# Kernel optimization log

Measured on AMD Instinct MI355X. Metric: run time of the kernel, lower is better.

The kernel has to match this reference:

```python
import jax, jax.numpy as jnp
import numpy as np

B = 1024      # batch of samples accumulated
F_DIM = 768   # backbone feature dim (ViT out_dim)
M = 512       # buffer_size (random projection width)
C = 100       # number of classes


def setup_inputs() -> dict:
    key = jax.random.key(0)
    k1, k2, k3 = jax.random.split(key, 3)
    X = jax.random.normal(k1, (B, F_DIM), dtype=jnp.float32)
    # RandomBuffer weight (fixed random projection), Linear-style init scale
    W = jax.random.normal(k2, (F_DIM, M), dtype=jnp.float32) / np.float32(np.sqrt(F_DIM))
    labels = jax.random.randint(k3, (B,), 0, C)  # argmax(Y, dim=1)
    return {"X": X, "W": W, "labels": labels}


def reference(X, W, labels):
    # RandomBuffer.forward: relu(X @ W) -> [B, M]
    feat = jax.nn.relu(X @ W)
    # per-sample outer product f^T f, scatter-added per class label
    outer = feat[:, :, None] * feat[:, None, :]          # [B, M, M]
    phi = jax.ops.segment_sum(outer, labels, num_segments=C)   # [C, M, M]
    mu = jax.ops.segment_sum(feat, labels, num_segments=C)     # [C, M]
    count = jax.ops.segment_sum(jnp.ones((B,), feat.dtype), labels, num_segments=C)  # [C]
    return phi, mu, count
```

## Files before the change

### kernel.cpp

```cpp
#include <hip/hip_runtime.h>

#define B_N    1024
#define F_DIMC 768
#define M_DIM  512
#define C_N    100
#define KHALF  (F_DIMC / 2)
#define NT2    (KHALF / 32)
#define NGEMM  512
#define NIDX   25

typedef float f32x4 __attribute__((ext_vector_type(4)));

__global__ __launch_bounds__(256) void gemm_index_kernel(
    const float* __restrict__ X, const float* __restrict__ W,
    const int* __restrict__ labels, float* __restrict__ part,
    int* __restrict__ counts, int* __restrict__ idx) {
  __shared__ float As[2][32][36];
  __shared__ float Bs[2][32][64];
  __shared__ int   lab[B_N];

  const int t = threadIdx.x;

  if (blockIdx.x >= NGEMM) {
    for (int i = t; i < B_N; i += 256) lab[i] = labels[i];
    __syncthreads();
    const int w    = t >> 6;
    const int lane = t & 63;
    const int c    = ((int)blockIdx.x - NGEMM) * 4 + w;
    if (c < C_N) {
      int base = 0;
      for (int ch = 0; ch < 16; ++ch) {
        const int j = ch * 64 + lane;
        const bool hit = (lab[j] == c);
        const unsigned long long mask = __ballot(hit);
        if (hit) {
          const int r = __popcll(mask & ((1ull << lane) - 1ull));
          idx[c * B_N + base + r] = j;
        }
        base += __popcll(mask);
      }
      if (lane == 0) counts[c] = base;
    }
    return;
  }

  const int kb   = (int)blockIdx.x >> 8;
  const int tile = (int)blockIdx.x & 255;
  const int bm = (tile >> 3) * 32;
  const int bn = (tile & 7) * 64;
  const int tx = t & 15;
  const int ty = t >> 4;

  const int ar  = t >> 3;
  const int akq = (t & 7) * 4;
  const int bk0 = t >> 4;
  const int bk1 = bk0 + 16;
  const int bnq = (t & 15) * 4;

  const float* __restrict__ Arow =
      X + (size_t)(bm + ar) * F_DIMC + kb * KHALF + akq;
  const float* __restrict__ Bcol =
      W + (size_t)kb * KHALF * M_DIM + bn + bnq;

  float4 pa  = *(const float4*)(Arow);
  float4 pb0 = *(const float4*)(Bcol + (size_t)bk0 * M_DIM);
  float4 pb1 = *(const float4*)(Bcol + (size_t)bk1 * M_DIM);

  float acc[2][4] = {};

  As[0][akq + 0][ar] = pa.x;
  As[0][akq + 1][ar] = pa.y;
  As[0][akq + 2][ar] = pa.z;
  As[0][akq + 3][ar] = pa.w;
  *(float4*)&Bs[0][bk0][bnq] = pb0;
  *(float4*)&Bs[0][bk1][bnq] = pb1;
  __syncthreads();

  for (int it = 0; it < NT2; ++it) {
    const int cur = it & 1;
    if (it + 1 < NT2) {
      const int k0 = (it + 1) * 32;
      pa  = *(const float4*)(Arow + k0);
      pb0 = *(const float4*)(Bcol + (size_t)(k0 + bk0) * M_DIM);
      pb1 = *(const float4*)(Bcol + (size_t)(k0 + bk1) * M_DIM);
    }
#pragma unroll
    for (int kk = 0; kk < 32; ++kk) {
      float2 av = *(const float2*)&As[cur][kk][ty * 2];
      float4 bv = *(const float4*)&Bs[cur][kk][tx * 4];
      acc[0][0] += av.x * bv.x;
      acc[0][1] += av.x * bv.y;
      acc[0][2] += av.x * bv.z;
      acc[0][3] += av.x * bv.w;
      acc[1][0] += av.y * bv.x;
      acc[1][1] += av.y * bv.y;
      acc[1][2] += av.y * bv.z;
      acc[1][3] += av.y * bv.w;
    }
    if (it + 1 < NT2) {
      const int nxt = cur ^ 1;
      As[nxt][akq + 0][ar] = pa.x;
      As[nxt][akq + 1][ar] = pa.y;
      As[nxt][akq + 2][ar] = pa.z;
      As[nxt][akq + 3][ar] = pa.w;
      *(float4*)&Bs[nxt][bk0][bnq] = pb0;
      *(float4*)&Bs[nxt][bk1][bnq] = pb1;
    }
    __syncthreads();
  }

  float* __restrict__ dst = part + (size_t)kb * B_N * M_DIM;
#pragma unroll
  for (int j = 0; j < 2; ++j) {
    float4 o = make_float4(acc[j][0], acc[j][1], acc[j][2], acc[j][3]);
    *(float4*)&dst[(size_t)(bm + ty * 2 + j) * M_DIM + bn + tx * 4] = o;
  }
}

__global__ __launch_bounds__(256, 4) void phi_mu_kernel(
    const float* __restrict__ p0, const float* __restrict__ p1,
    const int* __restrict__ counts, const int* __restrict__ idx,
    float* __restrict__ phi, float* __restrict__ mu,
    float* __restrict__ cnt_out) {
  const int c = blockIdx.y;
  const int n = counts[c];
  const int* __restrict__ id = idx + c * B_N;
  const int t = threadIdx.x;

  if (blockIdx.x == 16) {
    float2 acc = make_float2(0.f, 0.f);
    for (int s = 0; s < n; ++s) {
      const size_t o = (size_t)id[s] * M_DIM + t * 2;
      const float2 q0 = *(const float2*)&p0[o];
      const float2 q1 = *(const float2*)&p1[o];
      acc.x += fmaxf(q0.x + q1.x, 0.f);
      acc.y += fmaxf(q0.y + q1.y, 0.f);
    }
    *(float2*)&mu[(size_t)c * M_DIM + t * 2] = acc;
    if (t == 0) cnt_out[c] = (float)n;
    return;
  }

  const int px = (int)blockIdx.x;
  const int tr = t >> 6;
  const int tc = t & 63;

  __shared__ float F[16][M_DIM];

  float acc[8][8] = {};

  for (int s0 = 0; s0 < n; s0 += 16) {
    const int chunk  = min(16, n - s0);
    if (s0) __syncthreads();
    const int nslots = chunk << 7;
    for (int v = t; v < nslots; v += 256) {
      const int sl   = v >> 7;
      const int fp   = (v & 127) << 2;
      const size_t o = (size_t)id[s0 + sl] * M_DIM + fp;
      const float4 q0 = *(const float4*)&p0[o];
      const float4 q1 = *(const float4*)&p1[o];
      float4 f;
      f.x = fmaxf(q0.x + q1.x, 0.f);
      f.y = fmaxf(q0.y + q1.y, 0.f);
      f.z = fmaxf(q0.z + q1.z, 0.f);
      f.w = fmaxf(q0.w + q1.w, 0.f);
      *(float4*)&F[sl][fp] = f;
    }
    __syncthreads();
    for (int sl = 0; sl < chunk; ++sl) {
      const float4 a0 = *(const float4*)&F[sl][px * 32 + tr * 8];
      const float4 a1 = *(const float4*)&F[sl][px * 32 + tr * 8 + 4];
      const float4 b0 = *(const float4*)&F[sl][tc * 4];
      const float4 b1 = *(const float4*)&F[sl][256 + tc * 4];
      const float av[8] = {a0.x, a0.y, a0.z, a0.w, a1.x, a1.y, a1.z, a1.w};
      const float bv[8] = {b0.x, b0.y, b0.z, b0.w, b1.x, b1.y, b1.z, b1.w};
#pragma unroll
      for (int r = 0; r < 8; ++r)
#pragma unroll
        for (int q = 0; q < 8; ++q)
          acc[r][q] += av[r] * bv[q];
    }
  }

  float* __restrict__ out = phi + (size_t)c * M_DIM * M_DIM;
#pragma unroll
  for (int r = 0; r < 8; ++r) {
    const size_t row = (size_t)(px * 32 + tr * 8 + r) * M_DIM;
    const f32x4 o0 = {acc[r][0], acc[r][1], acc[r][2], acc[r][3]};
    const f32x4 o1 = {acc[r][4], acc[r][5], acc[r][6], acc[r][7]};
    __builtin_nontemporal_store(o0, (f32x4*)&out[row + tc * 4]);
    __builtin_nontemporal_store(o1, (f32x4*)&out[row + 256 + tc * 4]);
  }
}

extern "C" void kernel_launch(void* const* d_in, const int* in_sizes, int n_in,
                              void* d_out, int out_size, void* d_ws,
                              size_t ws_size, hipStream_t stream) {
  const float* X      = (const float*)d_in[0];
  const float* W      = (const float*)d_in[1];
  const int*   labels = (const int*)d_in[2];

  float* out = (float*)d_out;
  float* phi = out;
  float* mu  = out + (size_t)C_N * M_DIM * M_DIM;
  float* cnt = mu + (size_t)C_N * M_DIM;

  float* part   = (float*)d_ws;
  int*   counts = (int*)((char*)d_ws + (size_t)2 * B_N * M_DIM * sizeof(float));
  int*   idx    = counts + 128;

  hipLaunchKernelGGL(gemm_index_kernel, dim3(NGEMM + NIDX), dim3(256), 0,
                     stream, X, W, labels, part, counts, idx);
  hipLaunchKernelGGL(phi_mu_kernel, dim3(17, C_N), dim3(256), 0, stream,
                     part, part + (size_t)B_N * M_DIM, counts, idx,
                     phi, mu, cnt);
}
```

Baseline: 47.24 us.

## Merge split-K partials with atomics and enlarge phi blocks to 1024 threads

The two split-K GEMM halves now accumulate into a single zeroed buffer via float atomics, so the phi/mu kernel reads one partial instead of two. The buffer is cleared with a memset before the GEMM. The phi kernel is regrouped into 1024-thread blocks, each covering four 32-row strips, so every gathered sample chunk staged in LDS serves four times as many output rows. The nontemporal stores for phi are replaced by plain stores. This adds a memset, atomic traffic and fewer, larger blocks (5x100 grid), which may hurt occupancy and latency hiding.

New measurement: 60.39 us. 1.28x slower.

```diff
diff --git a/kernel.cpp b/kernel.cpp
--- a/kernel.cpp
+++ b/kernel.cpp
@@ -8,8 +8,6 @@
 #define NT2    (KHALF / 32)
 #define NGEMM  512
 #define NIDX   25
-
-typedef float f32x4 __attribute__((ext_vector_type(4)));
 
 __global__ __launch_bounds__(256) void gemm_index_kernel(
     const float* __restrict__ X, const float* __restrict__ W,
@@ -109,67 +107,64 @@
     __syncthreads();
   }
 
-  float* __restrict__ dst = part + (size_t)kb * B_N * M_DIM;
 #pragma unroll
   for (int j = 0; j < 2; ++j) {
-    float4 o = make_float4(acc[j][0], acc[j][1], acc[j][2], acc[j][3]);
-    *(float4*)&dst[(size_t)(bm + ty * 2 + j) * M_DIM + bn + tx * 4] = o;
+    float* __restrict__ d = part + (size_t)(bm + ty * 2 + j) * M_DIM + bn + tx * 4;
+    unsafeAtomicAdd(d + 0, acc[j][0]);
+    unsafeAtomicAdd(d + 1, acc[j][1]);
+    unsafeAtomicAdd(d + 2, acc[j][2]);
+    unsafeAtomicAdd(d + 3, acc[j][3]);
   }
 }
 
-__global__ __launch_bounds__(256, 4) void phi_mu_kernel(
-    const float* __restrict__ p0, const float* __restrict__ p1,
-    const int* __restrict__ counts, const int* __restrict__ idx,
-    float* __restrict__ phi, float* __restrict__ mu,
-    float* __restrict__ cnt_out) {
+__global__ __launch_bounds__(1024, 1) void phi_mu_kernel(
+    const float* __restrict__ part, const int* __restrict__ counts,
+    const int* __restrict__ idx, float* __restrict__ phi,
+    float* __restrict__ mu, float* __restrict__ cnt_out) {
   const int c = blockIdx.y;
   const int n = counts[c];
   const int* __restrict__ id = idx + c * B_N;
   const int t = threadIdx.x;
 
-  if (blockIdx.x == 16) {
-    float2 acc = make_float2(0.f, 0.f);
-    for (int s = 0; s < n; ++s) {
-      const size_t o = (size_t)id[s] * M_DIM + t * 2;
-      const float2 q0 = *(const float2*)&p0[o];
-      const float2 q1 = *(const float2*)&p1[o];
-      acc.x += fmaxf(q0.x + q1.x, 0.f);
-      acc.y += fmaxf(q0.y + q1.y, 0.f);
-    }
-    *(float2*)&mu[(size_t)c * M_DIM + t * 2] = acc;
+  if (blockIdx.x == 4) {
+    if (t < M_DIM) {
+      float a = 0.f;
+      for (int s = 0; s < n; ++s)
+        a += fmaxf(part[(size_t)id[s] * M_DIM + t], 0.f);
+      mu[(size_t)c * M_DIM + t] = a;
+    }
     if (t == 0) cnt_out[c] = (float)n;
     return;
   }
 
-  const int px = (int)blockIdx.x;
-  const int tr = t >> 6;
+  const int tp = t >> 8;
+  const int tr = (t >> 6) & 3;
   const int tc = t & 63;
+  const int prow = ((int)blockIdx.x * 4 + tp) * 32 + tr * 8;
 
   __shared__ float F[16][M_DIM];
 
   float acc[8][8] = {};
 
   for (int s0 = 0; s0 < n; s0 += 16) {
-    const int chunk  = min(16, n - s0);
+    const int chunk = min(16, n - s0);
     if (s0) __syncthreads();
     const int nslots = chunk << 7;
-    for (int v = t; v < nslots; v += 256) {
-      const int sl   = v >> 7;
-      const int fp   = (v & 127) << 2;
-      const size_t o = (size_t)id[s0 + sl] * M_DIM + fp;
-      const float4 q0 = *(const float4*)&p0[o];
-      const float4 q1 = *(const float4*)&p1[o];
+    for (int v = t; v < nslots; v += 1024) {
+      const int sl = v >> 7;
+      const int fp = (v & 127) << 2;
+      const float4 q = *(const float4*)&part[(size_t)id[s0 + sl] * M_DIM + fp];
       float4 f;
-      f.x = fmaxf(q0.x + q1.x, 0.f);
-      f.y = fmaxf(q0.y + q1.y, 0.f);
-      f.z = fmaxf(q0.z + q1.z, 0.f);
-      f.w = fmaxf(q0.w + q1.w, 0.f);
+      f.x = fmaxf(q.x, 0.f);
+      f.y = fmaxf(q.y, 0.f);
+      f.z = fmaxf(q.z, 0.f);
+      f.w = fmaxf(q.w, 0.f);
       *(float4*)&F[sl][fp] = f;
     }
     __syncthreads();
     for (int sl = 0; sl < chunk; ++sl) {
-      const float4 a0 = *(const float4*)&F[sl][px * 32 + tr * 8];
-      const float4 a1 = *(const float4*)&F[sl][px * 32 + tr * 8 + 4];
+      const float4 a0 = *(const float4*)&F[sl][prow];
+      const float4 a1 = *(const float4*)&F[sl][prow + 4];
       const float4 b0 = *(const float4*)&F[sl][tc * 4];
       const float4 b1 = *(const float4*)&F[sl][256 + tc * 4];
       const float av[8] = {a0.x, a0.y, a0.z, a0.w, a1.x, a1.y, a1.z, a1.w};
@@ -185,11 +180,11 @@
   float* __restrict__ out = phi + (size_t)c * M_DIM * M_DIM;
 #pragma unroll
   for (int r = 0; r < 8; ++r) {
-    const size_t row = (size_t)(px * 32 + tr * 8 + r) * M_DIM;
-    const f32x4 o0 = {acc[r][0], acc[r][1], acc[r][2], acc[r][3]};
-    const f32x4 o1 = {acc[r][4], acc[r][5], acc[r][6], acc[r][7]};
-    __builtin_nontemporal_store(o0, (f32x4*)&out[row + tc * 4]);
-    __builtin_nontemporal_store(o1, (f32x4*)&out[row + 256 + tc * 4]);
+    const size_t row = (size_t)(prow + r) * M_DIM;
+    *(float4*)&out[row + tc * 4] =
+        make_float4(acc[r][0], acc[r][1], acc[r][2], acc[r][3]);
+    *(float4*)&out[row + 256 + tc * 4] =
+        make_float4(acc[r][4], acc[r][5], acc[r][6], acc[r][7]);
   }
 }
 
@@ -206,12 +201,12 @@
   float* cnt = mu + (size_t)C_N * M_DIM;
 
   float* part   = (float*)d_ws;
-  int*   counts = (int*)((char*)d_ws + (size_t)2 * B_N * M_DIM * sizeof(float));
+  int*   counts = (int*)((char*)d_ws + (size_t)B_N * M_DIM * sizeof(float));
   int*   idx    = counts + 128;
 
+  hipMemsetAsync(part, 0, (size_t)B_N * M_DIM * sizeof(float), stream);
   hipLaunchKernelGGL(gemm_index_kernel, dim3(NGEMM + NIDX), dim3(256), 0,
                      stream, X, W, labels, part, counts, idx);
-  hipLaunchKernelGGL(phi_mu_kernel, dim3(17, C_N), dim3(256), 0, stream,
-                     part, part + (size_t)B_N * M_DIM, counts, idx,
-                     phi, mu, cnt);
+  hipLaunchKernelGGL(phi_mu_kernel, dim3(5, C_N), dim3(1024), 0, stream,
+                     part, counts, idx, phi, mu, cnt);
 }
```

## Split GEMM K four ways with 64x64 tiles and halve phi staging chunk

Applied to the files above, without the earlier changes.

The projection GEMM now splits K into four partial sums instead of two and uses 64x64 output tiles with a 4x4 register micro-tile per thread, keeping the block count at 512. The phi/mu kernel then reads and sums four partial buffers before the ReLU, and stages 8 samples per chunk instead of 16 to cut shared-memory use. The phi output stores change from nontemporal to ordinary stores. This gives more register reuse in the GEMM, but the second kernel reads twice as much partial data and synchronises more often.

New measurement: 48.83 us. 1.03x slower.

```diff
diff --git a/kernel.cpp b/kernel.cpp
--- a/kernel.cpp
+++ b/kernel.cpp
@@ -4,18 +4,17 @@
 #define F_DIMC 768
 #define M_DIM  512
 #define C_N    100
-#define KHALF  (F_DIMC / 2)
-#define NT2    (KHALF / 32)
+#define KSPLIT 4
+#define KPER   (F_DIMC / KSPLIT)
+#define NBK    (KPER / 32)
 #define NGEMM  512
 #define NIDX   25
-
-typedef float f32x4 __attribute__((ext_vector_type(4)));
 
 __global__ __launch_bounds__(256) void gemm_index_kernel(
     const float* __restrict__ X, const float* __restrict__ W,
     const int* __restrict__ labels, float* __restrict__ part,
     int* __restrict__ counts, int* __restrict__ idx) {
-  __shared__ float As[2][32][36];
+  __shared__ float As[2][32][68];
   __shared__ float Bs[2][32][64];
   __shared__ int   lab[B_N];
 
@@ -44,81 +43,88 @@
     return;
   }
 
-  const int kb   = (int)blockIdx.x >> 8;
-  const int tile = (int)blockIdx.x & 255;
-  const int bm = (tile >> 3) * 32;
+  const int kb   = (int)blockIdx.x >> 7;
+  const int tile = (int)blockIdx.x & 127;
+  const int bm = (tile >> 3) * 64;
   const int bn = (tile & 7) * 64;
-  const int tx = t & 15;
-  const int ty = t >> 4;
-
-  const int ar  = t >> 3;
-  const int akq = (t & 7) * 4;
-  const int bk0 = t >> 4;
-  const int bk1 = bk0 + 16;
-  const int bnq = (t & 15) * 4;
-
-  const float* __restrict__ Arow =
-      X + (size_t)(bm + ar) * F_DIMC + kb * KHALF + akq;
-  const float* __restrict__ Bcol =
-      W + (size_t)kb * KHALF * M_DIM + bn + bnq;
-
-  float4 pa  = *(const float4*)(Arow);
-  float4 pb0 = *(const float4*)(Bcol + (size_t)bk0 * M_DIM);
-  float4 pb1 = *(const float4*)(Bcol + (size_t)bk1 * M_DIM);
-
-  float acc[2][4] = {};
-
-  As[0][akq + 0][ar] = pa.x;
-  As[0][akq + 1][ar] = pa.y;
-  As[0][akq + 2][ar] = pa.z;
-  As[0][akq + 3][ar] = pa.w;
-  *(float4*)&Bs[0][bk0][bnq] = pb0;
-  *(float4*)&Bs[0][bk1][bnq] = pb1;
+  const int tr = t >> 4;
+  const int tc = t & 15;
+
+  const int ar0 = t >> 3,          akq0 = (t & 7) * 4;
+  const int ar1 = (t + 256) >> 3,  akq1 = (t & 7) * 4;
+  const int bkr0 = t >> 4,         bnq0 = (t & 15) * 4;
+  const int bkr1 = (t + 256) >> 4, bnq1 = (t & 15) * 4;
+
+  const float* __restrict__ Xb = X + (size_t)bm * F_DIMC + kb * KPER;
+  const float* __restrict__ Wb = W + (size_t)kb * KPER * M_DIM + bn;
+
+  float4 pa0 = *(const float4*)&Xb[(size_t)ar0 * F_DIMC + akq0];
+  float4 pa1 = *(const float4*)&Xb[(size_t)ar1 * F_DIMC + akq1];
+  float4 pb0 = *(const float4*)&Wb[(size_t)bkr0 * M_DIM + bnq0];
+  float4 pb1 = *(const float4*)&Wb[(size_t)bkr1 * M_DIM + bnq1];
+
+  float acc[4][4] = {};
+
+  As[0][akq0 + 0][ar0] = pa0.x;
+  As[0][akq0 + 1][ar0] = pa0.y;
+  As[0][akq0 + 2][ar0] = pa0.z;
+  As[0][akq0 + 3][ar0] = pa0.w;
+  As[0][akq1 + 0][ar1] = pa1.x;
+  As[0][akq1 + 1][ar1] = pa1.y;
+  As[0][akq1 + 2][ar1] = pa1.z;
+  As[0][akq1 + 3][ar1] = pa1.w;
+  *(float4*)&Bs[0][bkr0][bnq0] = pb0;
+  *(float4*)&Bs[0][bkr1][bnq1] = pb1;
   __syncthreads();
 
-  for (int it = 0; it < NT2; ++it) {
+  for (int it = 0; it < NBK; ++it) {
     const int cur = it & 1;
-    if (it + 1 < NT2) {
+    if (it + 1 < NBK) {
       const int k0 = (it + 1) * 32;
-      pa  = *(const float4*)(Arow + k0);
-      pb0 = *(const float4*)(Bcol + (size_t)(k0 + bk0) * M_DIM);
-      pb1 = *(const float4*)(Bcol + (size_t)(k0 + bk1) * M_DIM);
+      pa0 = *(const float4*)&Xb[(size_t)ar0 * F_DIMC + k0 + akq0];
+      pa1 = *(const float4*)&Xb[(size_t)ar1 * F_DIMC + k0 + akq1];
+      pb0 = *(const float4*)&Wb[(size_t)(k0 + bkr0) * M_DIM + bnq0];
+      pb1 = *(const float4*)&Wb[(size_t)(k0 + bkr1) * M_DIM + bnq1];
     }
 #pragma unroll
     for (int kk = 0; kk < 32; ++kk) {
-      float2 av = *(const float2*)&As[cur][kk][ty * 2];
-      float4 bv = *(const float4*)&Bs[cur][kk][tx * 4];
-      acc[0][0] += av.x * bv.x;
-      acc[0][1] += av.x * bv.y;
-      acc[0][2] += av.x * bv.z;
-      acc[0][3] += av.x * bv.w;
-      acc[1][0] += av.y * bv.x;
-      acc[1][1] += av.y * bv.y;
-      acc[1][2] += av.y * bv.z;
-      acc[1][3] += av.y * bv.w;
-    }
-    if (it + 1 < NT2) {
+      const float4 a = *(const float4*)&As[cur][kk][tr * 4];
+      const float4 b = *(const float4*)&Bs[cur][kk][tc * 4];
+      const float av[4] = {a.x, a.y, a.z, a.w};
+      const float bv[4] = {b.x, b.y, b.z, b.w};
+#pragma unroll
+      for (int j = 0; j < 4; ++j)
+#pragma unroll
+        for (int q = 0; q < 4; ++q)
+          acc[j][q] += av[j] * bv[q];
+    }
+    if (it + 1 < NBK) {
       const int nxt = cur ^ 1;
-      As[nxt][akq + 0][ar] = pa.x;
-      As[nxt][akq + 1][ar] = pa.y;
-      As[nxt][akq + 2][ar] = pa.z;
-      As[nxt][akq + 3][ar] = pa.w;
-      *(float4*)&Bs[nxt][bk0][bnq] = pb0;
-      *(float4*)&Bs[nxt][bk1][bnq] = pb1;
+      As[nxt][akq0 + 0][ar0] = pa0.x;
+      As[nxt][akq0 + 1][ar0] = pa0.y;
+      As[nxt][akq0 + 2][ar0] = pa0.z;
+      As[nxt][akq0 + 3][ar0] = pa0.w;
+      As[nxt][akq1 + 0][ar1] = pa1.x;
+      As[nxt][akq1 + 1][ar1] = pa1.y;
+      As[nxt][akq1 + 2][ar1] = pa1.z;
+      As[nxt][akq1 + 3][ar1] = pa1.w;
+      *(float4*)&Bs[nxt][bkr0][bnq0] = pb0;
+      *(float4*)&Bs[nxt][bkr1][bnq1] = pb1;
     }
     __syncthreads();
   }
 
   float* __restrict__ dst = part + (size_t)kb * B_N * M_DIM;
 #pragma unroll
-  for (int j = 0; j < 2; ++j) {
-    float4 o = make_float4(acc[j][0], acc[j][1], acc[j][2], acc[j][3]);
-    *(float4*)&dst[(size_t)(bm + ty * 2 + j) * M_DIM + bn + tx * 4] = o;
+  for (int j = 0; j < 4; ++j) {
+    *(float4*)&dst[(size_t)(bm + tr * 4 + j) * M_DIM + bn + tc * 4] =
+        make_float4(acc[j][0], acc[j][1], acc[j][2], acc[j][3]);
   }
 }
 
 __global__ __launch_bounds__(256, 4) void phi_mu_kernel(
     const float* __restrict__ p0, const float* __restrict__ p1,
+    const float* __restrict__ p2, const float* __restrict__ p3,
     const int* __restrict__ counts, const int* __restrict__ idx,
     float* __restrict__ phi, float* __restrict__ mu,
     float* __restrict__ cnt_out) {
@@ -133,8 +139,10 @@
       const size_t o = (size_t)id[s] * M_DIM + t * 2;
       const float2 q0 = *(const float2*)&p0[o];
       const float2 q1 = *(const float2*)&p1[o];
-      acc.x += fmaxf(q0.x + q1.x, 0.f);
-      acc.y += fmaxf(q0.y + q1.y, 0.f);
+      const float2 q2 = *(const float2*)&p2[o];
+      const float2 q3 = *(const float2*)&p3[o];
+      acc.x += fmaxf(((q0.x + q1.x) + q2.x) + q3.x, 0.f);
+      acc.y += fmaxf(((q0.y + q1.y) + q2.y) + q3.y, 0.f);
     }
     *(float2*)&mu[(size_t)c * M_DIM + t * 2] = acc;
     if (t == 0) cnt_out[c] = (float)n;
@@ -145,12 +153,12 @@
   const int tr = t >> 6;
   const int tc = t & 63;
 
-  __shared__ float F[16][M_DIM];
+  __shared__ float F[8][M_DIM];
 
   float acc[8][8] = {};
 
-  for (int s0 = 0; s0 < n; s0 += 16) {
-    const int chunk  = min(16, n - s0);
+  for (int s0 = 0; s0 < n; s0 += 8) {
+    const int chunk  = min(8, n - s0);
     if (s0) __syncthreads();
     const int nslots = chunk << 7;
     for (int v = t; v < nslots; v += 256) {
@@ -159,11 +167,13 @@
       const size_t o = (size_t)id[s0 + sl] * M_DIM + fp;
       const float4 q0 = *(const float4*)&p0[o];
       const float4 q1 = *(const float4*)&p1[o];
+      const float4 q2 = *(const float4*)&p2[o];
+      const float4 q3 = *(const float4*)&p3[o];
       float4 f;
-      f.x = fmaxf(q0.x + q1.x, 0.f);
-      f.y = fmaxf(q0.y + q1.y, 0.f);
-      f.z = fmaxf(q0.z + q1.z, 0.f);
-      f.w = fmaxf(q0.w + q1.w, 0.f);
+      f.x = fmaxf(((q0.x + q1.x) + q2.x) + q3.x, 0.f);
+      f.y = fmaxf(((q0.y + q1.y) + q2.y) + q3.y, 0.f);
+      f.z = fmaxf(((q0.z + q1.z) + q2.z) + q3.z, 0.f);
+      f.w = fmaxf(((q0.w + q1.w) + q2.w) + q3.w, 0.f);
       *(float4*)&F[sl][fp] = f;
     }
     __syncthreads();
@@ -186,10 +196,10 @@
 #pragma unroll
   for (int r = 0; r < 8; ++r) {
     const size_t row = (size_t)(px * 32 + tr * 8 + r) * M_DIM;
-    const f32x4 o0 = {acc[r][0], acc[r][1], acc[r][2], acc[r][3]};
-    const f32x4 o1 = {acc[r][4], acc[r][5], acc[r][6], acc[r][7]};
-    __builtin_nontemporal_store(o0, (f32x4*)&out[row + tc * 4]);
-    __builtin_nontemporal_store(o1, (f32x4*)&out[row + 256 + tc * 4]);
+    *(float4*)&out[row + tc * 4] =
+        make_float4(acc[r][0], acc[r][1], acc[r][2], acc[r][3]);
+    *(float4*)&out[row + 256 + tc * 4] =
+        make_float4(acc[r][4], acc[r][5], acc[r][6], acc[r][7]);
   }
 }
 
@@ -206,12 +216,15 @@
   float* cnt = mu + (size_t)C_N * M_DIM;
 
   float* part   = (float*)d_ws;
-  int*   counts = (int*)((char*)d_ws + (size_t)2 * B_N * M_DIM * sizeof(float));
+  int*   counts = (int*)((char*)d_ws +
+                         (size_t)KSPLIT * B_N * M_DIM * sizeof(float));
   int*   idx    = counts + 128;
+
+  const size_t seg = (size_t)B_N * M_DIM;
 
   hipLaunchKernelGGL(gemm_index_kernel, dim3(NGEMM + NIDX), dim3(256), 0,
                      stream, X, W, labels, part, counts, idx);
   hipLaunchKernelGGL(phi_mu_kernel, dim3(17, C_N), dim3(256), 0, stream,
-                     part, part + (size_t)B_N * M_DIM, counts, idx,
-                     phi, mu, cnt);
+                     part, part + seg, part + 2 * seg, part + 3 * seg,
+                     counts, idx, phi, mu, cnt);
 }
```

## Use split-bf16 MFMA for feature GEMM and drop split-K partials

Applied to the files above, without the earlier changes.

The FP32 scalar-FMA GEMM for relu(X@W) is replaced by bf16 MFMA 16x16x32 instructions. Each operand is split into hi and lo bf16 parts and three MFMAs are issued to recover near-fp32 accuracy. The split-K over two halves is removed: each block now computes the full K for a 32x32 tile and writes relu'd features directly. This removes the second partial buffer and the add+relu work in the phi/mu kernel. The cost is extra conversion work when staging tiles, a slight loss of precision from dropping the lo*lo term, and fewer output values per block.

Measured after the change: 42.69 us. -9.6%, faster.

```diff
diff --git a/kernel.cpp b/kernel.cpp
--- a/kernel.cpp
+++ b/kernel.cpp
@@ -4,29 +4,39 @@
 #define F_DIMC 768
 #define M_DIM  512
 #define C_N    100
-#define KHALF  (F_DIMC / 2)
-#define NT2    (KHALF / 32)
+#define KSTEP  32
+#define NSTEP  (F_DIMC / KSTEP)
 #define NGEMM  512
 #define NIDX   25
 
 typedef float f32x4 __attribute__((ext_vector_type(4)));
+typedef short s16x8 __attribute__((ext_vector_type(8)));
+
+__device__ __forceinline__ unsigned int f2bf(float x) {
+  unsigned int u = __builtin_bit_cast(unsigned int, x);
+  return (u + 0x7fffu + ((u >> 16) & 1u)) >> 16;
+}
+__device__ __forceinline__ float bf2f(unsigned int h) {
+  return __builtin_bit_cast(float, h << 16);
+}
 
 __global__ __launch_bounds__(256) void gemm_index_kernel(
     const float* __restrict__ X, const float* __restrict__ W,
-    const int* __restrict__ labels, float* __restrict__ part,
+    const int* __restrict__ labels, float* __restrict__ feat,
     int* __restrict__ counts, int* __restrict__ idx) {
-  __shared__ float As[2][32][36];
-  __shared__ float Bs[2][32][64];
-  __shared__ int   lab[B_N];
+  __shared__ unsigned short Ah[2][32][40], Al[2][32][40];
+  __shared__ unsigned short Bh[2][32][40], Bl[2][32][40];
+  __shared__ int lab[B_N];
 
   const int t = threadIdx.x;
-
-  if (blockIdx.x >= NGEMM) {
+  const int b = (int)blockIdx.x;
+
+  if (b >= NGEMM) {
     for (int i = t; i < B_N; i += 256) lab[i] = labels[i];
     __syncthreads();
     const int w    = t >> 6;
     const int lane = t & 63;
-    const int c    = ((int)blockIdx.x - NGEMM) * 4 + w;
+    const int c    = (b - NGEMM) * 4 + w;
     if (c < C_N) {
       int base = 0;
       for (int ch = 0; ch < 16; ++ch) {
@@ -44,84 +54,101 @@
     return;
   }
 
-  const int kb   = (int)blockIdx.x >> 8;
-  const int tile = (int)blockIdx.x & 255;
-  const int bm = (tile >> 3) * 32;
-  const int bn = (tile & 7) * 64;
-  const int tx = t & 15;
-  const int ty = t >> 4;
-
-  const int ar  = t >> 3;
-  const int akq = (t & 7) * 4;
-  const int bk0 = t >> 4;
-  const int bk1 = bk0 + 16;
-  const int bnq = (t & 15) * 4;
-
-  const float* __restrict__ Arow =
-      X + (size_t)(bm + ar) * F_DIMC + kb * KHALF + akq;
-  const float* __restrict__ Bcol =
-      W + (size_t)kb * KHALF * M_DIM + bn + bnq;
-
-  float4 pa  = *(const float4*)(Arow);
-  float4 pb0 = *(const float4*)(Bcol + (size_t)bk0 * M_DIM);
-  float4 pb1 = *(const float4*)(Bcol + (size_t)bk1 * M_DIM);
-
-  float acc[2][4] = {};
-
-  As[0][akq + 0][ar] = pa.x;
-  As[0][akq + 1][ar] = pa.y;
-  As[0][akq + 2][ar] = pa.z;
-  As[0][akq + 3][ar] = pa.w;
-  *(float4*)&Bs[0][bk0][bnq] = pb0;
-  *(float4*)&Bs[0][bk1][bnq] = pb1;
+  const int bm = (b >> 4) * 32;
+  const int bn = (b & 15) * 32;
+
+  const bool isX = (t < 128);
+  const int xr = t >> 2;
+  const int xk = (t & 3) * 8;
+  const int uu = isX ? 0 : (t - 128);
+  const int wk = (uu >> 3) * 2;
+  const int wc = (uu & 7) * 4;
+
+  const float* __restrict__ Xp = X + (size_t)(bm + xr) * F_DIMC + xk;
+  const float* __restrict__ Wp = W + (size_t)wk * M_DIM + bn + wc;
+
+  const int lane = t & 63;
+  const int wv   = t >> 6;
+  const int m0 = (wv & 1) * 16;
+  const int n0 = (wv >> 1) * 16;
+  const int fr = lane & 15;
+  const int fq = (lane >> 4) * 8;
+
+  f32x4 acc = {0.f, 0.f, 0.f, 0.f};
+
+  float4 ra0, ra1, rb0, rb1;
+  if (isX) {
+    ra0 = *(const float4*)(Xp);
+    ra1 = *(const float4*)(Xp + 4);
+  } else {
+    rb0 = *(const float4*)(Wp);
+    rb1 = *(const float4*)(Wp + M_DIM);
+  }
+
+  auto STAGE = [&](int buf) {
+    if (isX) {
+      const float v[8] = {ra0.x, ra0.y, ra0.z, ra0.w,
+                          ra1.x, ra1.y, ra1.z, ra1.w};
+      s16x8 hv, lv;
+#pragma unroll
+      for (int j = 0; j < 8; ++j) {
+        const unsigned int hb = f2bf(v[j]);
+        hv[j] = (short)hb;
+        lv[j] = (short)f2bf(v[j] - bf2f(hb));
+      }
+      *(s16x8*)&Ah[buf][xr][xk] = hv;
+      *(s16x8*)&Al[buf][xr][xk] = lv;
+    } else {
+      const float a[4] = {rb0.x, rb0.y, rb0.z, rb0.w};
+      const float d[4] = {rb1.x, rb1.y, rb1.z, rb1.w};
+#pragma unroll
+      for (int i = 0; i < 4; ++i) {
+        const unsigned int ha = f2bf(a[i]), hd = f2bf(d[i]);
+        const unsigned int la = f2bf(a[i] - bf2f(ha));
+        const unsigned int ld = f2bf(d[i] - bf2f(hd));
+        *(unsigned int*)&Bh[buf][wc + i][wk] = ha | (hd << 16);
+        *(unsigned int*)&Bl[buf][wc + i][wk] = la | (ld << 16);
+      }
+    }
+  };
+
+  STAGE(0);
   __syncthreads();
 
-  for (int it = 0; it < NT2; ++it) {
+  for (int it = 0; it < NSTEP; ++it) {
     const int cur = it & 1;
-    if (it + 1 < NT2) {
-      const int k0 = (it + 1) * 32;
-      pa  = *(const float4*)(Arow + k0);
-      pb0 = *(const float4*)(Bcol + (size_t)(k0 + bk0) * M_DIM);
-      pb1 = *(const float4*)(Bcol + (size_t)(k0 + bk1) * M_DIM);
-    }
-#pragma unroll
-    for (int kk = 0; kk < 32; ++kk) {
-      float2 av = *(const float2*)&As[cur][kk][ty * 2];
-      float4 bv = *(const float4*)&Bs[cur][kk][tx * 4];
-      acc[0][0] += av.x * bv.x;
-      acc[0][1] += av.x * bv.y;
-      acc[0][2] += av.x * bv.z;
-      acc[0][3] += av.x * bv.w;
-      acc[1][0] += av.y * bv.x;
-      acc[1][1] += av.y * bv.y;
-      acc[1][2] += av.y * bv.z;
-      acc[1][3] += av.y * bv.w;
-    }
-    if (it + 1 < NT2) {
-      const int nxt = cur ^ 1;
-      As[nxt][akq + 0][ar] = pa.x;
-      As[nxt][akq + 1][ar] = pa.y;
-      As[nxt][akq + 2][ar] = pa.z;
-      As[nxt][akq + 3][ar] = pa.w;
-      *(float4*)&Bs[nxt][bk0][bnq] = pb0;
-      *(float4*)&Bs[nxt][bk1][bnq] = pb1;
-    }
+    if (it + 1 < NSTEP) {
+      const int k0 = (it + 1) * KSTEP;
+      if (isX) {
+        ra0 = *(const float4*)(Xp + k0);
+        ra1 = *(const float4*)(Xp + k0 + 4);
+      } else {
+        rb0 = *(const float4*)(Wp + (size_t)k0 * M_DIM);
+        rb1 = *(const float4*)(Wp + (size_t)(k0 + 1) * M_DIM);
+      }
+    }
+    const s16x8 ah = *(const s16x8*)&Ah[cur][m0 + fr][fq];
+    const s16x8 al = *(const s16x8*)&Al[cur][m0 + fr][fq];
+    const s16x8 bh = *(const s16x8*)&Bh[cur][n0 + fr][fq];
+    const s16x8 bl = *(const s16x8*)&Bl[cur][n0 + fr][fq];
+    acc = __builtin_amdgcn_mfma_f32_16x16x32_bf16(ah, bh, acc, 0, 0, 0);
+    acc = __builtin_amdgcn_mfma_f32_16x16x32_bf16(al, bh, acc, 0, 0, 0);
+    acc = __builtin_amdgcn_mfma_f32_16x16x32_bf16(ah, bl, acc, 0, 0, 0);
+    if (it + 1 < NSTEP) STAGE(cur ^ 1);
     __syncthreads();
   }
 
-  float* __restrict__ dst = part + (size_t)kb * B_N * M_DIM;
-#pragma unroll
-  for (int j = 0; j < 2; ++j) {
-    float4 o = make_float4(acc[j][0], acc[j][1], acc[j][2], acc[j][3]);
-    *(float4*)&dst[(size_t)(bm + ty * 2 + j) * M_DIM + bn + tx * 4] = o;
-  }
+  const int r0 = (lane >> 4) * 4;
+#pragma unroll
+  for (int r = 0; r < 4; ++r)
+    feat[(size_t)(bm + m0 + r0 + r) * M_DIM + bn + n0 + fr] =
+        fmaxf(acc[r], 0.0f);
 }
 
 __global__ __launch_bounds__(256, 4) void phi_mu_kernel(
-    const float* __restrict__ p0, const float* __restrict__ p1,
-    const int* __restrict__ counts, const int* __restrict__ idx,
-    float* __restrict__ phi, float* __restrict__ mu,
-    float* __restrict__ cnt_out) {
+    const float* __restrict__ feat, const int* __restrict__ counts,
+    const int* __restrict__ idx, float* __restrict__ phi,
+    float* __restrict__ mu, float* __restrict__ cnt_out) {
   const int c = blockIdx.y;
   const int n = counts[c];
   const int* __restrict__ id = idx + c * B_N;
@@ -130,11 +157,9 @@
   if (blockIdx.x == 16) {
     float2 acc = make_float2(0.f, 0.f);
     for (int s = 0; s < n; ++s) {
-      const size_t o = (size_t)id[s] * M_DIM + t * 2;
-      const float2 q0 = *(const float2*)&p0[o];
-      const float2 q1 = *(const float2*)&p1[o];
-      acc.x += fmaxf(q0.x + q1.x, 0.f);
-      acc.y += fmaxf(q0.y + q1.y, 0.f);
+      const float2 q = *(const float2*)&feat[(size_t)id[s] * M_DIM + t * 2];
+      acc.x += q.x;
+      acc.y += q.y;
     }
     *(float2*)&mu[(size_t)c * M_DIM + t * 2] = acc;
     if (t == 0) cnt_out[c] = (float)n;
@@ -154,17 +179,10 @@
     if (s0) __syncthreads();
     const int nslots = chunk << 7;
     for (int v = t; v < nslots; v += 256) {
-      const int sl   = v >> 7;
-      const int fp   = (v & 127) << 2;
-      const size_t o = (size_t)id[s0 + sl] * M_DIM + fp;
-      const float4 q0 = *(const float4*)&p0[o];
-      const float4 q1 = *(const float4*)&p1[o];
-      float4 f;
-      f.x = fmaxf(q0.x + q1.x, 0.f);
-      f.y = fmaxf(q0.y + q1.y, 0.f);
-      f.z = fmaxf(q0.z + q1.z, 0.f);
-      f.w = fmaxf(q0.w + q1.w, 0.f);
-      *(float4*)&F[sl][fp] = f;
+      const int sl = v >> 7;
+      const int fp = (v & 127) << 2;
+      *(float4*)&F[sl][fp] =
+          *(const float4*)&feat[(size_t)id[s0 + sl] * M_DIM + fp];
     }
     __syncthreads();
     for (int sl = 0; sl < chunk; ++sl) {
@@ -205,13 +223,12 @@
   float* mu  = out + (size_t)C_N * M_DIM * M_DIM;
   float* cnt = mu + (size_t)C_N * M_DIM;
 
-  float* part   = (float*)d_ws;
-  int*   counts = (int*)((char*)d_ws + (size_t)2 * B_N * M_DIM * sizeof(float));
+  float* feat   = (float*)d_ws;
+  int*   counts = (int*)((char*)d_ws + (size_t)B_N * M_DIM * sizeof(float));
   int*   idx    = counts + 128;
 
   hipLaunchKernelGGL(gemm_index_kernel, dim3(NGEMM + NIDX), dim3(256), 0,
-                     stream, X, W, labels, part, counts, idx);
+                     stream, X, W, labels, feat, counts, idx);
   hipLaunchKernelGGL(phi_mu_kernel, dim3(17, C_N), dim3(256), 0, stream,
-                     part, part + (size_t)B_N * M_DIM, counts, idx,
-                     phi, mu, cnt);
-}
+                     feat, counts, idx, phi, mu, cnt);
+}
```
